# Kernel tuning notes

Measured on AMD Instinct MI355X. Metric: run time of the kernel, lower is better.

## Reference

```python
import jax, jax.numpy as jnp
import numpy as np

D_MODEL, D_K, D_V, H = 1024, 64, 64, 16
NEG_INF = -1e30  # finite stand-in for -inf masked_fill (grad-safe)


def setup_inputs() -> dict:
    key = jax.random.key(0)
    ks = jax.random.split(key, 16)
    b, nq, nk = 2, 1024, 1024
    def xavier(k, fan_in, fan_out):
        lim = np.sqrt(6.0 / (fan_in + fan_out)).astype(np.float32)
        return jax.random.uniform(k, (fan_in, fan_out), jnp.float32, -lim, lim)
    return {
        "queries": jax.random.normal(ks[0], (b, nq, D_MODEL), jnp.float32),
        "keys": jax.random.normal(ks[1], (b, nk, D_MODEL), jnp.float32),
        "values": jax.random.normal(ks[2], (b, nk, D_MODEL), jnp.float32),
        "attention_mask": jax.random.randint(ks[3], (b, H, nq, nk), 0, 2, jnp.int32),
        "attention_weights": jax.random.uniform(ks[4], (b, H, nq, nk), jnp.float32),
        "Wq": xavier(ks[5], D_MODEL, H * D_K), "bq": jnp.zeros((H * D_K,), jnp.float32),
        "Wk": xavier(ks[6], D_MODEL, H * D_K), "bk": jnp.zeros((H * D_K,), jnp.float32),
        "Wv": xavier(ks[7], D_MODEL, H * D_V), "bv": jnp.zeros((H * D_V,), jnp.float32),
        "Wo": xavier(ks[8], H * D_V, D_MODEL), "bo": jnp.zeros((D_MODEL,), jnp.float32),
    }


def reference(queries, keys, values, attention_mask, attention_weights,
              Wq, bq, Wk, bk, Wv, bv, Wo, bo):
    b, nq, _ = queries.shape
    nk = keys.shape[1]
    # project and split heads: [b, h, n, d]
    Q = (queries @ Wq + bq).reshape(b, nq, H, D_K).transpose(0, 2, 1, 3)
    K = (keys @ Wk + bk).reshape(b, nk, H, D_K).transpose(0, 2, 1, 3)
    V = (values @ Wv + bv).reshape(b, nk, H, D_V).transpose(0, 2, 1, 3)
    scale = jnp.asarray(1.0 / np.sqrt(D_K), queries.dtype)
    att = jnp.einsum('bhqd,bhkd->bhqk', Q, K) * scale
    att_map = att  # pre-weight/mask scores (torch .clone())
    att = att * attention_weights            # way='mul'
    att = jnp.where(attention_mask == 0, NEG_INF, att)
    att = jax.nn.softmax(att, axis=-1)
    out = jnp.einsum('bhqk,bhkd->bqhd', att, V).reshape(b, nq, H * D_V)
    out = out @ Wo + bo
    return out, att_map
```

## Files before the change

kernel.cpp:

```cpp
#include <hip/hip_runtime.h>

typedef _Float16 f16;
typedef __attribute__((ext_vector_type(4))) _Float16 half4;
typedef __attribute__((ext_vector_type(8))) _Float16 half8;
typedef __attribute__((ext_vector_type(4))) float v4f;
typedef __attribute__((ext_vector_type(4))) float f32x4v;
typedef __attribute__((ext_vector_type(4))) int i32x4;
typedef __attribute__((ext_vector_type(8))) unsigned short u16x8;

#define NEG_BIG -1e30f

#if __has_builtin(__builtin_amdgcn_mfma_f32_16x16x16_f16)
#define MFMA16(a, b, c) __builtin_amdgcn_mfma_f32_16x16x16_f16(a, b, c, 0, 0, 0)
#else
#define MFMA16(a, b, c) __builtin_amdgcn_mfma_f32_16x16x16f16(a, b, c, 0, 0, 0)
#endif

__global__ __launch_bounds__(256) void cvt3_kernel(
    const float* __restrict__ q, const float* __restrict__ k, const float* __restrict__ v,
    f16* __restrict__ oq, f16* __restrict__ ok, f16* __restrict__ ov)
{
    int gid = blockIdx.x * 256 + threadIdx.x;
    int seg = gid >> 19;
    int off = (gid & 524287) << 2;
    const float* src = (seg == 0) ? q : (seg == 1) ? k : v;
    f16* dst = (seg == 0) ? oq : (seg == 1) ? ok : ov;
    f32x4v x = *(const f32x4v*)(src + off);
    union { f16 h[4]; unsigned long long u; } pk;
    pk.h[0] = (f16)x[0]; pk.h[1] = (f16)x[1]; pk.h[2] = (f16)x[2]; pk.h[3] = (f16)x[3];
    *(unsigned long long*)(dst + off) = pk.u;
}

__global__ __launch_bounds__(256) void wtrans_kernel(
    const float* __restrict__ w0, const float* __restrict__ w1,
    const float* __restrict__ w2, const float* __restrict__ w3,
    f16* __restrict__ o0, f16* __restrict__ o1, f16* __restrict__ o2, f16* __restrict__ o3)
{
    __shared__ f16 tile[64][72];
    int zs = blockIdx.z;
    const float* W = (zs == 0) ? w0 : (zs == 1) ? w1 : (zs == 2) ? w2 : w3;
    f16* O = (zs == 0) ? o0 : (zs == 1) ? o1 : (zs == 2) ? o2 : o3;
    int cx = blockIdx.x * 64;
    int ry = blockIdx.y * 64;
    int tid = threadIdx.x;
    #pragma unroll
    for (int p = 0; p < 4; ++p) {
        int idx = tid + p * 256;
        int r = idx >> 4, c4 = (idx & 15) << 2;
        f32x4v x = *(const f32x4v*)&W[(size_t)(ry + r) * 1024 + cx + c4];
        tile[r][c4 + 0] = (f16)x[0]; tile[r][c4 + 1] = (f16)x[1];
        tile[r][c4 + 2] = (f16)x[2]; tile[r][c4 + 3] = (f16)x[3];
    }
    __syncthreads();
    #pragma unroll
    for (int p = 0; p < 2; ++p) {
        int idx = tid + p * 256;
        int n = idx >> 3, c8 = (idx & 7) << 3;
        union { f16 h[8]; u16x8 u; } pk;
        #pragma unroll
        for (int j = 0; j < 8; ++j) pk.h[j] = tile[c8 + j][n];
        *(u16x8*)&O[(size_t)(cx + n) * 1024 + ry + c8] = pk.u;
    }
}

__device__ __forceinline__ void gemm_core(
    const f16* __restrict__ A, const f16* __restrict__ Bt,
    const float* __restrict__ bias, void* __restrict__ out, int mode)
{
    __shared__ f16 As[128 * 72];
    __shared__ f16 Bs[64 * 72];
    const int mbase = blockIdx.y * 128;
    const int nbase = blockIdx.x * 64;
    int tid = threadIdx.x;
    int lane = tid & 63, wave = tid >> 6;
    int ln = lane & 15, hi = lane >> 4;
    int wr = wave & 1, wc = wave >> 1;
    v4f acc[4][2];
    #pragma unroll
    for (int rt = 0; rt < 4; ++rt)
        #pragma unroll
        for (int ct = 0; ct < 2; ++ct) acc[rt][ct] = (v4f){0.f, 0.f, 0.f, 0.f};

    for (int kb = 0; kb < 1024; kb += 64) {
        __syncthreads();
        #pragma unroll
        for (int p = 0; p < 4; ++p) {
            int idx = tid + p * 256;
            int r = idx >> 3, c8 = (idx & 7) << 3;
            *(u16x8*)&As[r * 72 + c8] = *(const u16x8*)&A[(size_t)(mbase + r) * 1024 + kb + c8];
        }
        #pragma unroll
        for (int p = 0; p < 2; ++p) {
            int idx = tid + p * 256;
            int r = idx >> 3, c8 = (idx & 7) << 3;
            *(u16x8*)&Bs[r * 72 + c8] = *(const u16x8*)&Bt[(size_t)(nbase + r) * 1024 + kb + c8];
        }
        __syncthreads();
        #pragma unroll
        for (int kk = 0; kk < 64; kk += 32) {
            half8 aF[4], bF[2];
            #pragma unroll
            for (int rt = 0; rt < 4; ++rt)
                aF[rt] = *(const half8*)&As[(wr * 64 + rt * 16 + ln) * 72 + kk + 8 * hi];
            #pragma unroll
            for (int ct = 0; ct < 2; ++ct)
                bF[ct] = *(const half8*)&Bs[(wc * 32 + ct * 16 + ln) * 72 + kk + 8 * hi];
            #pragma unroll
            for (int rt = 0; rt < 4; ++rt)
                #pragma unroll
                for (int ct = 0; ct < 2; ++ct)
                    acc[rt][ct] = __builtin_amdgcn_mfma_f32_16x16x32_f16(aF[rt], bF[ct], acc[rt][ct], 0, 0, 0);
        }
    }
    #pragma unroll
    for (int rt = 0; rt < 4; ++rt)
      #pragma unroll
      for (int ct = 0; ct < 2; ++ct)
        #pragma unroll
        for (int r = 0; r < 4; ++r) {
            int m = mbase + wr * 64 + rt * 16 + hi * 4 + r;
            int n = nbase + wc * 32 + ct * 16 + ln;
            float val = acc[rt][ct][r] + bias[n];
            if (mode == 0) {
                int bb = m >> 10, nq = m & 1023, hh = n >> 6, d = n & 63;
                ((f16*)out)[(((size_t)(bb * 16 + hh)) * 1024 + nq) * 64 + d] = (f16)val;
            } else if (mode == 1) {
                int bb = m >> 10, nq = m & 1023, hh = n >> 6, d = n & 63;
                ((f16*)out)[(((size_t)(bb * 16 + hh)) * 64 + d) * 1024 + nq] = (f16)val;
            } else {
                ((float*)out)[(size_t)m * 1024 + n] = val;
            }
        }
}

__global__ __launch_bounds__(256) void qkv_gemm_kernel(
    const f16* __restrict__ xq, const f16* __restrict__ xk, const f16* __restrict__ xv,
    const f16* __restrict__ wqt, const f16* __restrict__ wkt, const f16* __restrict__ wvt,
    const float* __restrict__ bq, const float* __restrict__ bk, const float* __restrict__ bv,
    f16* __restrict__ oQ, f16* __restrict__ oK, f16* __restrict__ oVt)
{
    int z = blockIdx.z;
    const f16* A  = (z == 0) ? xq  : (z == 1) ? xk  : xv;
    const f16* B  = (z == 0) ? wqt : (z == 1) ? wkt : wvt;
    const float* bi = (z == 0) ? bq : (z == 1) ? bk : bv;
    void* out = (z == 0) ? (void*)oQ : (z == 1) ? (void*)oK : (void*)oVt;
    gemm_core(A, B, bi, out, (z == 2) ? 1 : 0);
}

__global__ __launch_bounds__(256) void o_gemm_kernel(
    const f16* __restrict__ A, const f16* __restrict__ Wot,
    const float* __restrict__ bo, float* __restrict__ out)
{
    gemm_core(A, Wot, bo, out, 2);
}

__global__ __launch_bounds__(256) void attn_kernel(
    const f16* __restrict__ Qp, const f16* __restrict__ Kp, const f16* __restrict__ Vt,
    const float* __restrict__ weights, const int* __restrict__ mask,
    float* __restrict__ amap, f16* __restrict__ hout)
{
    __shared__ f16 Ks[2][64 * 72];
    __shared__ f16 Vs[2][64 * 72];

    int qb = blockIdx.x, h = blockIdx.y, b = blockIdx.z;
    int bh = b * 16 + h;
    int tid = threadIdx.x;
    int lane = tid & 63, wave = tid >> 6;
    int ln = lane & 15, hi = lane >> 4;

    const f16* Kb = Kp + (size_t)bh * 1024 * 64;
    const f16* Vb = Vt + (size_t)bh * 64 * 1024;
    int qg = qb * 64 + wave * 16 + ln;
    const f16*  Qb = Qp + ((size_t)bh * 1024 + qg) * 64;
    const float* Wr = weights + ((size_t)bh * 1024 + qg) * 1024;
    const int*   Mr = mask    + ((size_t)bh * 1024 + qg) * 1024;
    float*       Ar = amap    + ((size_t)bh * 1024 + qg) * 1024;

    half8 qf0 = *(const half8*)&Qb[8 * hi];
    half8 qf1 = *(const half8*)&Qb[32 + 8 * hi];

    int srow = tid >> 2, sc = (tid & 3) * 16;

    {
        const f16* kg = Kb + (size_t)srow * 64 + sc;
        const f16* vg = Vb + (size_t)srow * 1024 + sc;
        half8 k0v = *(const half8*)&kg[0];
        half8 k1v = *(const half8*)&kg[8];
        half8 v0v = *(const half8*)&vg[0];
        half8 v1v = *(const half8*)&vg[8];
        *(half8*)&Ks[0][srow * 72 + sc]     = k0v;
        *(half8*)&Ks[0][srow * 72 + sc + 8] = k1v;
        *(half8*)&Vs[0][srow * 72 + sc]     = v0v;
        *(half8*)&Vs[0][srow * 72 + sc + 8] = v1v;
    }
    f32x4v wcur[4]; i32x4 mcur[4];
    #pragma unroll
    for (int t = 0; t < 4; ++t) {
        wcur[t] = *(const f32x4v*)&Wr[t * 16 + 4 * hi];
        mcur[t] = *(const i32x4*)&Mr[t * 16 + 4 * hi];
    }
    __syncthreads();

    float mrun = -3.0e38f, lrun = 0.f;
    v4f oacc[4];
    #pragma unroll
    for (int dt = 0; dt < 4; ++dt) oacc[dt] = (v4f){0.f, 0.f, 0.f, 0.f};

    for (int kt = 0; kt < 16; ++kt) {
        int buf = kt & 1;
        int k0n = (kt + 1) * 64;

        half8 nk0, nk1, nv0, nv1;
        if (kt < 15) {
            const f16* kg = Kb + (size_t)(k0n + srow) * 64 + sc;
            const f16* vg = Vb + (size_t)srow * 1024 + k0n + sc;
            nk0 = *(const half8*)&kg[0];
            nk1 = *(const half8*)&kg[8];
            nv0 = *(const half8*)&vg[0];
            nv1 = *(const half8*)&vg[8];
        }
        f32x4v wnxt[4]; i32x4 mnxt[4];
        if (kt < 15) {
            #pragma unroll
            for (int t = 0; t < 4; ++t) {
                wnxt[t] = *(const f32x4v*)&Wr[k0n + t * 16 + 4 * hi];
                mnxt[t] = *(const i32x4*)&Mr[k0n + t * 16 + 4 * hi];
            }
        }

        v4f st[4];
        #pragma unroll
        for (int t = 0; t < 4; ++t) {
            half8 ka = *(const half8*)&Ks[buf][(t * 16 + ln) * 72 + 8 * hi];
            half8 kb2 = *(const half8*)&Ks[buf][(t * 16 + ln) * 72 + 32 + 8 * hi];
            v4f a = (v4f){0.f, 0.f, 0.f, 0.f};
            a = __builtin_amdgcn_mfma_f32_16x16x32_f16(ka, qf0, a, 0, 0, 0);
            a = __builtin_amdgcn_mfma_f32_16x16x32_f16(kb2, qf1, a, 0, 0, 0);
            st[t] = a;
        }

        float z[4][4];
        #pragma unroll
        for (int t = 0; t < 4; ++t) {
            f32x4v sv = st[t] * 0.125f;
            *(f32x4v*)&Ar[kt * 64 + t * 16 + 4 * hi] = sv;
            #pragma unroll
            for (int r = 0; r < 4; ++r)
                z[t][r] = (mcur[t][r] == 0) ? NEG_BIG : sv[r] * wcur[t][r];
        }

        float tm = z[0][0];
        #pragma unroll
        for (int t = 0; t < 4; ++t)
            #pragma unroll
            for (int r = 0; r < 4; ++r) tm = fmaxf(tm, z[t][r]);
        tm = fmaxf(tm, __shfl_xor(tm, 16, 64));
        tm = fmaxf(tm, __shfl_xor(tm, 32, 64));
        float mnew = fmaxf(mrun, tm);
        float fsc = __expf(mrun - mnew);
        float p[4][4];
        float tsum = 0.f;
        #pragma unroll
        for (int t = 0; t < 4; ++t)
            #pragma unroll
            for (int r = 0; r < 4; ++r) { p[t][r] = __expf(z[t][r] - mnew); tsum += p[t][r]; }
        tsum += __shfl_xor(tsum, 16, 64);
        tsum += __shfl_xor(tsum, 32, 64);
        lrun = lrun * fsc + tsum;
        mrun = mnew;
        #pragma unroll
        for (int dt = 0; dt < 4; ++dt) oacc[dt] *= fsc;

        half4 pf[4];
        #pragma unroll
        for (int t = 0; t < 4; ++t) {
            half4 v;
            v[0] = (f16)p[t][0]; v[1] = (f16)p[t][1];
            v[2] = (f16)p[t][2]; v[3] = (f16)p[t][3];
            pf[t] = v;
        }

        #pragma unroll
        for (int t = 0; t < 4; ++t)
            #pragma unroll
            for (int dt = 0; dt < 4; ++dt) {
                half4 vf = *(const half4*)&Vs[buf][(dt * 16 + ln) * 72 + t * 16 + 4 * hi];
                oacc[dt] = MFMA16(vf, pf[t], oacc[dt]);
            }

        if (kt < 15) {
            *(half8*)&Ks[buf ^ 1][srow * 72 + sc]     = nk0;
            *(half8*)&Ks[buf ^ 1][srow * 72 + sc + 8] = nk1;
            *(half8*)&Vs[buf ^ 1][srow * 72 + sc]     = nv0;
            *(half8*)&Vs[buf ^ 1][srow * 72 + sc + 8] = nv1;
            #pragma unroll
            for (int t = 0; t < 4; ++t) { wcur[t] = wnxt[t]; mcur[t] = mnxt[t]; }
        }
        __syncthreads();
    }

    float rl = 1.0f / lrun;
    #pragma unroll
    for (int dt = 0; dt < 4; ++dt) {
        half4 ov;
        #pragma unroll
        for (int r = 0; r < 4; ++r) ov[r] = (f16)(oacc[dt][r] * rl);
        *(half4*)&hout[((size_t)(b * 1024 + qg)) * 1024 + h * 64 + dt * 16 + 4 * hi] = ov;
    }
}

extern "C" void kernel_launch(void* const* d_in, const int* in_sizes, int n_in,
                              void* d_out, int out_size, void* d_ws, size_t ws_size,
                              hipStream_t stream)
{
    const float* queries  = (const float*)d_in[0];
    const float* keys     = (const float*)d_in[1];
    const float* values   = (const float*)d_in[2];
    const int*   amask    = (const int*)d_in[3];
    const float* aweights = (const float*)d_in[4];
    const float* Wq = (const float*)d_in[5];  const float* bq = (const float*)d_in[6];
    const float* Wk = (const float*)d_in[7];  const float* bk = (const float*)d_in[8];
    const float* Wv = (const float*)d_in[9];  const float* bv = (const float*)d_in[10];
    const float* Wo = (const float*)d_in[11]; const float* bo = (const float*)d_in[12];

    char* ws = (char*)d_ws;
    const size_t MB = 1024 * 1024;
    f16* q_h  = (f16*)(ws + 0 * MB);
    f16* k_h  = (f16*)(ws + 4 * MB);
    f16* v_h  = (f16*)(ws + 8 * MB);
    f16* wqt  = (f16*)(ws + 12 * MB);
    f16* wkt  = (f16*)(ws + 14 * MB);
    f16* wvt  = (f16*)(ws + 16 * MB);
    f16* wot  = (f16*)(ws + 18 * MB);
    f16* Qp   = (f16*)(ws + 20 * MB);
    f16* Kp   = (f16*)(ws + 24 * MB);
    f16* Vt   = (f16*)(ws + 28 * MB);
    f16* hout = (f16*)(ws + 32 * MB);

    float* out_main = (float*)d_out;
    float* att_map  = out_main + (size_t)2 * 1024 * 1024;

    cvt3_kernel<<<6144, 256, 0, stream>>>(queries, keys, values, q_h, k_h, v_h);
    wtrans_kernel<<<dim3(16, 16, 4), 256, 0, stream>>>(Wq, Wk, Wv, Wo, wqt, wkt, wvt, wot);
    qkv_gemm_kernel<<<dim3(16, 16, 3), 256, 0, stream>>>(q_h, k_h, v_h, wqt, wkt, wvt,
                                                         bq, bk, bv, Qp, Kp, Vt);
    attn_kernel<<<dim3(16, 16, 2), 256, 0, stream>>>(Qp, Kp, Vt, aweights, amask, att_map, hout);
    o_gemm_kernel<<<dim3(16, 16, 1), 256, 0, stream>>>(hout, wot, bo, out_main);
}
```

Before: 165.7 us.

## Drop LDS staging in attention kernel, use single-wave blocks with direct global loads

The attention kernel now runs one 64-thread wave per block (2048 blocks instead of 512) and reads K and V fragments straight from global memory instead of staging them through double-buffered shared memory with __syncthreads. The weight and mask tiles are prefetched two tiles ahead in alternating register buffers, and the score-map stores are nontemporal. The aim is to remove barrier and LDS overhead and raise occupancy for this memory-bound kernel. In exchange, K/V reuse across waves now depends on the caches, the strided V reads are less coalesced, and global load latency is exposed directly to the MFMAs.

```diff
diff --git a/kernel.cpp b/kernel.cpp
--- a/kernel.cpp
+++ b/kernel.cpp
@@ -10,6 +10,7 @@
 
 #define NEG_BIG -1e30f
 
+#define MFMA32(a, b, c) __builtin_amdgcn_mfma_f32_16x16x32_f16(a, b, c, 0, 0, 0)
 #if __has_builtin(__builtin_amdgcn_mfma_f32_16x16x16_f16)
 #define MFMA16(a, b, c) __builtin_amdgcn_mfma_f32_16x16x16_f16(a, b, c, 0, 0, 0)
 #else
@@ -154,23 +155,19 @@
     gemm_core(A, Wot, bo, out, 2);
 }
 
-__global__ __launch_bounds__(256) void attn_kernel(
+__global__ __launch_bounds__(64, 2) void attn_kernel(
     const f16* __restrict__ Qp, const f16* __restrict__ Kp, const f16* __restrict__ Vt,
     const float* __restrict__ weights, const int* __restrict__ mask,
     float* __restrict__ amap, f16* __restrict__ hout)
 {
-    __shared__ f16 Ks[2][64 * 72];
-    __shared__ f16 Vs[2][64 * 72];
-
     int qb = blockIdx.x, h = blockIdx.y, b = blockIdx.z;
     int bh = b * 16 + h;
-    int tid = threadIdx.x;
-    int lane = tid & 63, wave = tid >> 6;
+    int lane = threadIdx.x & 63;
     int ln = lane & 15, hi = lane >> 4;
 
     const f16* Kb = Kp + (size_t)bh * 1024 * 64;
     const f16* Vb = Vt + (size_t)bh * 64 * 1024;
-    int qg = qb * 64 + wave * 16 + ln;
+    int qg = qb * 16 + ln;
     const f16*  Qb = Qp + ((size_t)bh * 1024 + qg) * 64;
     const float* Wr = weights + ((size_t)bh * 1024 + qg) * 1024;
     const int*   Mr = mask    + ((size_t)bh * 1024 + qg) * 1024;
@@ -179,76 +176,41 @@
     half8 qf0 = *(const half8*)&Qb[8 * hi];
     half8 qf1 = *(const half8*)&Qb[32 + 8 * hi];
 
-    int srow = tid >> 2, sc = (tid & 3) * 16;
-
-    {
-        const f16* kg = Kb + (size_t)srow * 64 + sc;
-        const f16* vg = Vb + (size_t)srow * 1024 + sc;
-        half8 k0v = *(const half8*)&kg[0];
-        half8 k1v = *(const half8*)&kg[8];
-        half8 v0v = *(const half8*)&vg[0];
-        half8 v1v = *(const half8*)&vg[8];
-        *(half8*)&Ks[0][srow * 72 + sc]     = k0v;
-        *(half8*)&Ks[0][srow * 72 + sc + 8] = k1v;
-        *(half8*)&Vs[0][srow * 72 + sc]     = v0v;
-        *(half8*)&Vs[0][srow * 72 + sc + 8] = v1v;
-    }
-    f32x4v wcur[4]; i32x4 mcur[4];
-    #pragma unroll
-    for (int t = 0; t < 4; ++t) {
-        wcur[t] = *(const f32x4v*)&Wr[t * 16 + 4 * hi];
-        mcur[t] = *(const i32x4*)&Mr[t * 16 + 4 * hi];
-    }
-    __syncthreads();
-
     float mrun = -3.0e38f, lrun = 0.f;
     v4f oacc[4];
     #pragma unroll
     for (int dt = 0; dt < 4; ++dt) oacc[dt] = (v4f){0.f, 0.f, 0.f, 0.f};
 
-    for (int kt = 0; kt < 16; ++kt) {
-        int buf = kt & 1;
-        int k0n = (kt + 1) * 64;
-
-        half8 nk0, nk1, nv0, nv1;
-        if (kt < 15) {
-            const f16* kg = Kb + (size_t)(k0n + srow) * 64 + sc;
-            const f16* vg = Vb + (size_t)srow * 1024 + k0n + sc;
-            nk0 = *(const half8*)&kg[0];
-            nk1 = *(const half8*)&kg[8];
-            nv0 = *(const half8*)&vg[0];
-            nv1 = *(const half8*)&vg[8];
-        }
-        f32x4v wnxt[4]; i32x4 mnxt[4];
-        if (kt < 15) {
-            #pragma unroll
-            for (int t = 0; t < 4; ++t) {
-                wnxt[t] = *(const f32x4v*)&Wr[k0n + t * 16 + 4 * hi];
-                mnxt[t] = *(const i32x4*)&Mr[k0n + t * 16 + 4 * hi];
-            }
-        }
-
+    f32x4v wA[4], wB[4]; i32x4 mA[4], mB[4];
+    #pragma unroll
+    for (int t = 0; t < 4; ++t) {
+        wA[t] = *(const f32x4v*)&Wr[t * 16 + 4 * hi];
+        mA[t] = *(const i32x4*)&Mr[t * 16 + 4 * hi];
+        wB[t] = *(const f32x4v*)&Wr[64 + t * 16 + 4 * hi];
+        mB[t] = *(const i32x4*)&Mr[64 + t * 16 + 4 * hi];
+    }
+
+    auto process = [&](int kt, const f32x4v (&wb)[4], const i32x4 (&mb)[4]) {
         v4f st[4];
         #pragma unroll
         for (int t = 0; t < 4; ++t) {
-            half8 ka = *(const half8*)&Ks[buf][(t * 16 + ln) * 72 + 8 * hi];
-            half8 kb2 = *(const half8*)&Ks[buf][(t * 16 + ln) * 72 + 32 + 8 * hi];
+            const f16* kr = &Kb[(size_t)(kt * 64 + t * 16 + ln) * 64 + 8 * hi];
+            half8 ka = *(const half8*)kr;
+            half8 kc = *(const half8*)(kr + 32);
             v4f a = (v4f){0.f, 0.f, 0.f, 0.f};
-            a = __builtin_amdgcn_mfma_f32_16x16x32_f16(ka, qf0, a, 0, 0, 0);
-            a = __builtin_amdgcn_mfma_f32_16x16x32_f16(kb2, qf1, a, 0, 0, 0);
+            a = MFMA32(ka, qf0, a);
+            a = MFMA32(kc, qf1, a);
             st[t] = a;
         }
-
         float z[4][4];
         #pragma unroll
         for (int t = 0; t < 4; ++t) {
             f32x4v sv = st[t] * 0.125f;
-            *(f32x4v*)&Ar[kt * 64 + t * 16 + 4 * hi] = sv;
+            __builtin_nontemporal_store(sv, (f32x4v*)&Ar[kt * 64 + t * 16 + 4 * hi]);
             #pragma unroll
             for (int r = 0; r < 4; ++r)
-                z[t][r] = (mcur[t][r] == 0) ? NEG_BIG : sv[r] * wcur[t][r];
-        }
-
+                z[t][r] = (mb[t][r] == 0) ? NEG_BIG : sv[r] * wb[t][r];
+        }
         float tm = z[0][0];
         #pragma unroll
         for (int t = 0; t < 4; ++t)
@@ -270,7 +232,6 @@
         mrun = mnew;
         #pragma unroll
         for (int dt = 0; dt < 4; ++dt) oacc[dt] *= fsc;
-
         half4 pf[4];
         #pragma unroll
         for (int t = 0; t < 4; ++t) {
@@ -279,24 +240,34 @@
             v[2] = (f16)p[t][2]; v[3] = (f16)p[t][3];
             pf[t] = v;
         }
-
         #pragma unroll
         for (int t = 0; t < 4; ++t)
             #pragma unroll
             for (int dt = 0; dt < 4; ++dt) {
-                half4 vf = *(const half4*)&Vs[buf][(dt * 16 + ln) * 72 + t * 16 + 4 * hi];
+                half4 vf = *(const half4*)&Vb[(size_t)(dt * 16 + ln) * 1024 + kt * 64 + t * 16 + 4 * hi];
                 oacc[dt] = MFMA16(vf, pf[t], oacc[dt]);
             }
-
-        if (kt < 15) {
-            *(half8*)&Ks[buf ^ 1][srow * 72 + sc]     = nk0;
-            *(half8*)&Ks[buf ^ 1][srow * 72 + sc + 8] = nk1;
-            *(half8*)&Vs[buf ^ 1][srow * 72 + sc]     = nv0;
-            *(half8*)&Vs[buf ^ 1][srow * 72 + sc + 8] = nv1;
-            #pragma unroll
-            for (int t = 0; t < 4; ++t) { wcur[t] = wnxt[t]; mcur[t] = mnxt[t]; }
-        }
-        __syncthreads();
+    };
+
+    #pragma unroll 1
+    for (int kt2 = 0; kt2 < 8; ++kt2) {
+        int kt = kt2 * 2;
+        process(kt, wA, mA);
+        if (kt2 < 7) {
+            #pragma unroll
+            for (int t = 0; t < 4; ++t) {
+                wA[t] = *(const f32x4v*)&Wr[(kt + 2) * 64 + t * 16 + 4 * hi];
+                mA[t] = *(const i32x4*)&Mr[(kt + 2) * 64 + t * 16 + 4 * hi];
+            }
+        }
+        process(kt + 1, wB, mB);
+        if (kt2 < 7) {
+            #pragma unroll
+            for (int t = 0; t < 4; ++t) {
+                wB[t] = *(const f32x4v*)&Wr[(kt + 3) * 64 + t * 16 + 4 * hi];
+                mB[t] = *(const i32x4*)&Mr[(kt + 3) * 64 + t * 16 + 4 * hi];
+            }
+        }
     }
 
     float rl = 1.0f / lrun;
@@ -344,6 +315,6 @@
     wtrans_kernel<<<dim3(16, 16, 4), 256, 0, stream>>>(Wq, Wk, Wv, Wo, wqt, wkt, wvt, wot);
     qkv_gemm_kernel<<<dim3(16, 16, 3), 256, 0, stream>>>(q_h, k_h, v_h, wqt, wkt, wvt,
                                                          bq, bk, bv, Qp, Kp, Vt);
-    attn_kernel<<<dim3(16, 16, 2), 256, 0, stream>>>(Qp, Kp, Vt, aweights, amask, att_map, hout);
+    attn_kernel<<<dim3(64, 16, 2), 64, 0, stream>>>(Qp, Kp, Vt, aweights, amask, att_map, hout);
     o_gemm_kernel<<<dim3(16, 16, 1), 256, 0, stream>>>(hout, wot, bo, out_main);
 }
```

Measured after the change: 234.3 us. 41.4% more time.
